# Kernel tuning notes

Hardware: AMD Instinct MI355X
Metric: run time of the kernel (lower is better)

Reference implementation:

```python
import jax, jax.numpy as jnp
import numpy as np

VX, VY = 0.16, 0.16
X_OFFSET = VX / 2 + 0.0      # vx/2 + offset[0]
Y_OFFSET = VY / 2 + (-39.68) # vy/2 + offset[1]
BN_EPS = 1e-5
V, P, C_IN, C_OUT = 40000, 32, 4, 64


def setup_inputs() -> dict:
    key = jax.random.key(0)
    k0, k1, k2, k3 = jax.random.split(key, 4)
    voxels = jax.random.normal(k0, (V, P, C_IN), dtype=jnp.float32)
    num_point_per_voxel = jnp.maximum(
        jax.random.randint(k1, (V,), 0, P + 1), 1).astype(jnp.int32)
    coors = jax.random.randint(k2, (V, 2), 0, 400).astype(jnp.int32)
    W = jax.random.normal(k3, (C_OUT, C_IN + 5), dtype=jnp.float32) * 0.1
    gamma = jnp.ones((C_OUT,), dtype=jnp.float32)
    beta = jnp.zeros((C_OUT,), dtype=jnp.float32)
    return {"voxels": voxels, "num_point_per_voxel": num_point_per_voxel,
            "coors": coors, "W": W, "gamma": gamma, "beta": beta}


def reference(voxels, num_point_per_voxel, coors, W, gamma, beta):
    npts = num_point_per_voxel.astype(voxels.dtype)  # [V]
    xyz = voxels[:, :, :3]
    # cluster offset: subtract per-pillar mean of valid points
    points_mean = jnp.sum(xyz, axis=1, keepdims=True) / npts[:, None, None]
    f_cluster = xyz - points_mean  # [V, P, 3]
    # pillar-center offset
    cx = coors[:, 0].astype(voxels.dtype) * VX + X_OFFSET  # [V]
    cy = coors[:, 1].astype(voxels.dtype) * VY + Y_OFFSET
    f_center = jnp.stack([voxels[:, :, 0] - cx[:, None],
                          voxels[:, :, 1] - cy[:, None]], axis=-1)  # [V, P, 2]
    features = jnp.concatenate([voxels, f_cluster, f_center], axis=-1)  # [V, P, 9]
    # zero out padded points
    point_ids = jnp.arange(P, dtype=jnp.int32)[None, :]
    mask = (num_point_per_voxel[:, None] > point_ids).astype(features.dtype)
    features = features * mask[:, :, None]
    # 1x1 conv == per-point linear: [V, P, 9] x [64, 9] -> [V, P, 64]
    x = jnp.einsum('vpc,oc->vpo', features, W)
    # BatchNorm1d (train mode): stats over (voxel, point) dims per channel
    mean = jnp.mean(x, axis=(0, 1))
    var = jnp.var(x, axis=(0, 1))
    x = (x - mean) * jax.lax.rsqrt(var + BN_EPS) * gamma + beta
    x = jax.nn.relu(x)
    # max over points -> [V, 64]
    return jnp.max(x, axis=1)
```

## Files before the change

kernel.cpp:

```cpp
#include <hip/hip_runtime.h>
#include <hip/hip_bf16.h>

#define V_N   40000
#define P_N   32
#define NTOT  (V_N * P_N)
#define VXc   0.16f
#define VYc   0.16f
#define XOFF  0.08f
#define YOFF  (-39.6f)
#define BN_EPS 1e-5f

#define SBLK  250
#define PBLK  2500
#define NSHARD 8
#define CNT_BYTES  (54 * NSHARD * 32 * 4)
#define MEANS_OFF  57344
#define CY_OFF     (MEANS_OFF + V_N * 16)

#define FOR_S(X) X(0) X(1) X(2) X(3) X(4) X(5) X(6) X(7) X(8)
#define FOR_M(X) \
  X(0,0) X(0,1) X(0,2) X(0,3) X(0,4) X(0,5) X(0,6) X(0,7) X(0,8) \
  X(1,1) X(1,2) X(1,3) X(1,4) X(1,5) X(1,6) X(1,7) X(1,8) \
  X(2,2) X(2,3) X(2,4) X(2,5) X(2,6) X(2,7) X(2,8) \
  X(3,3) X(3,4) X(3,5) X(3,6) X(3,7) X(3,8) \
  X(4,4) X(4,5) X(4,6) X(4,7) X(4,8) \
  X(5,5) X(5,6) X(5,7) X(5,8) \
  X(6,6) X(6,7) X(6,8) \
  X(7,7) X(7,8) \
  X(8,8)

__device__ __forceinline__ float wave_sum(float x) {
#pragma unroll
    for (int m = 1; m < 64; m <<= 1) x += __shfl_xor(x, m, 64);
    return x;
}

__device__ __forceinline__ float rdlane(float x, int l) {
    return __uint_as_float(__builtin_amdgcn_readlane(__float_as_uint(x), l));
}

#define DECL_S(i)   float S##i = 0.f;
#define DECL_M(i,j) float M##i##_##j = 0.f;
#define ACC_S(i)    S##i += f##i;
#define ACC_M(i,j)  M##i##_##j = fmaf(f##i, f##j, M##i##_##j);
#define RED_S(i)    S##i = wave_sum(S##i);
#define RED_M(i,j)  M##i##_##j = wave_sum(M##i##_##j);
#define ST_S(i)     r[k++] = S##i;
#define ST_M(i,j)   r[k++] = M##i##_##j;

#define STAT_BODY(q, v)                                                       \
        {                                                                     \
            float sx = q.x, sy = q.y, sz = q.z;                               \
            _Pragma("unroll")                                                 \
            for (int m = 1; m < 32; m <<= 1) {                                \
                sx += __shfl_xor(sx, m, 64);                                  \
                sy += __shfl_xor(sy, m, 64);                                  \
                sz += __shfl_xor(sz, m, 64);                                  \
            }                                                                 \
            const int   npts = npts_arr[v];                                   \
            const float inv  = 1.f / (float)npts;                             \
            const float mx = sx * inv, my = sy * inv, mz = sz * inv;          \
            const float cx = (float)coors[2 * (v)]     * VXc + XOFF;          \
            const float cy = (float)coors[2 * (v) + 1] * VYc + YOFF;          \
            if (p == 0) { means[v] = make_float4(mx, my, mz, cx);             \
                          cyv[v] = cy; }                                      \
            const float g  = (p < npts) ? 1.f : 0.f;                          \
            const float f0 = q.x * g;                                         \
            const float f1 = q.y * g;                                         \
            const float f2 = q.z * g;                                         \
            const float f3 = q.w * g;                                         \
            const float f4 = (q.x - mx) * g;                                  \
            const float f5 = (q.y - my) * g;                                  \
            const float f6 = (q.z - mz) * g;                                  \
            const float f7 = (q.x - cx) * g;                                  \
            const float f8 = (q.y - cy) * g;                                  \
            FOR_S(ACC_S)                                                      \
            FOR_M(ACC_M)                                                      \
        }

__global__ __launch_bounds__(256) void stats_kernel(
    const float4* __restrict__ voxels,
    const int*    __restrict__ npts_arr,
    const int*    __restrict__ coors,
    float*        __restrict__ ws)
{
    float*  cnt   = ws;
    float4* means = (float4*)((char*)ws + MEANS_OFF);
    float*  cyv   = (float*)((char*)ws + CY_OFF);

    const int lane = threadIdx.x & 63;
    const int p    = lane & 31;
    const int half = lane >> 5;
    const int gw   = (blockIdx.x * 256 + threadIdx.x) >> 6;
    const int nw   = (SBLK * 256) >> 6;

    FOR_S(DECL_S)
    FOR_M(DECL_M)

    for (int vb = gw * 4; vb < V_N; vb += nw * 4) {
        const int vA = vb + half;
        const int vB = vb + 2 + half;
        float4 q1 = voxels[(size_t)vA * P_N + p];
        float4 q2 = voxels[(size_t)vB * P_N + p];
        STAT_BODY(q1, vA)
        STAT_BODY(q2, vB)
    }

    FOR_S(RED_S)
    FOR_M(RED_M)

    __shared__ float red[4][54];
    const int wib = threadIdx.x >> 6;
    if (lane == 0) {
        float* r = red[wib];
        int k = 0;
        FOR_S(ST_S)
        FOR_M(ST_M)
    }
    __syncthreads();
    if (threadIdx.x < 54) {
        float s = red[0][threadIdx.x] + red[1][threadIdx.x]
                + red[2][threadIdx.x] + red[3][threadIdx.x];
        atomicAdd(&cnt[(threadIdx.x * NSHARD + (blockIdx.x & (NSHARD - 1))) * 32], s);
    }
}

__global__ __launch_bounds__(256) void pfn_kernel(
    const float4* __restrict__ voxels,
    const int*    __restrict__ npts_arr,
    const float*  __restrict__ W,
    const float*  __restrict__ gamma,
    const float*  __restrict__ beta,
    const float*  __restrict__ ws,
    float*        __restrict__ out)
{
    const float*  cnt   = ws;
    const float4* means = (const float4*)((const char*)ws + MEANS_OFF);
    const float*  cyv   = (const float*)((const char*)ws + CY_OFF);

    __shared__ float stc[54];
    __shared__ float affs[10][64];

    const int lane = threadIdx.x & 63;
    const int wib  = threadIdx.x >> 6;

    if (threadIdx.x < 54) {
        float s = 0.f;
#pragma unroll
        for (int sh = 0; sh < NSHARD; ++sh)
            s += cnt[(threadIdx.x * NSHARD + sh) * 32];
        stc[threadIdx.x] = s;
    }
    __syncthreads();
    if (threadIdx.x < 64) {
        const int o = threadIdx.x;
        float w[9];
#pragma unroll
        for (int c = 0; c < 9; ++c) w[c] = W[o * 9 + c];

        const float invN = 1.f / (float)NTOT;
        float mean = 0.f;
#pragma unroll
        for (int c = 0; c < 9; ++c) mean = fmaf(w[c], stc[c], mean);
        mean *= invN;

        float ex2 = 0.f;
        int k = 9;
#pragma unroll
        for (int i = 0; i < 9; ++i)
#pragma unroll
            for (int j = i; j < 9; ++j) {
                const float coef = (i == j) ? 1.f : 2.f;
                ex2 = fmaf(coef * w[i] * w[j], stc[k], ex2);
                ++k;
            }
        ex2 *= invN;
        const float var   = ex2 - mean * mean;
        const float scale = gamma[o] * rsqrtf(var + BN_EPS);
        const float bias  = fmaf(-mean, scale, beta[o]);

        affs[0][o] = (w[0] + w[4] + w[7]) * scale;
        affs[1][o] = (w[1] + w[5] + w[8]) * scale;
        affs[2][o] = (w[2] + w[6]) * scale;
        affs[3][o] =  w[3] * scale;
        affs[4][o] =  w[4] * scale;
        affs[5][o] =  w[5] * scale;
        affs[6][o] =  w[6] * scale;
        affs[7][o] =  w[7] * scale;
        affs[8][o] =  w[8] * scale;
        affs[9][o] =  bias;
    }
    __syncthreads();

    const float a0   = affs[0][lane];
    const float a1   = affs[1][lane];
    const float a2   = affs[2][lane];
    const float a3   = affs[3][lane];
    const float u4   = affs[4][lane];
    const float u5   = affs[5][lane];
    const float u6   = affs[6][lane];
    const float u7   = affs[7][lane];
    const float u8   = affs[8][lane];
    const float bias = affs[9][lane];

    const int gwave = blockIdx.x * 4 + wib;

#define DOT(P_, OFS_) \
    fmaf(rdlane(q.x, (P_) + (OFS_)), a0, \
    fmaf(rdlane(q.y, (P_) + (OFS_)), a1, \
    fmaf(rdlane(q.z, (P_) + (OFS_)), a2, \
         rdlane(q.w, (P_) + (OFS_)) * a3)))

#pragma unroll
    for (int it = 0; it < 2; ++it) {
        const int vA = gwave * 4 + it * 2;
        const int vB = vA + 1;

        const int vv = vA + (lane >> 5);
        const float4 q = voxels[(size_t)vv * P_N + (lane & 31)];

        const int nA = __builtin_amdgcn_readfirstlane(npts_arr[vA]);
        const int nB = __builtin_amdgcn_readfirstlane(npts_arr[vB]);

        const float4 mA = means[vA];
        const float4 mB = means[vB];
        const float cyA = cyv[vA];
        const float cyB = cyv[vB];

        const float bA = -fmaf(mA.x, u4, fmaf(mA.y, u5, fmaf(mA.z, u6,
                           fmaf(mA.w, u7, cyA * u8))));
        const float bB = -fmaf(mB.x, u4, fmaf(mB.y, u5, fmaf(mB.z, u6,
                           fmaf(mB.w, u7, cyB * u8))));

        float e0 = -3.4e38f, e1 = -3.4e38f;
        {
            int pp = 0;
            for (; pp + 1 < nA; pp += 2) {
                const float d0 = DOT(pp, 0);
                const float d1 = DOT(pp + 1, 0);
                e0 = fmaxf(e0, d0);
                e1 = fmaxf(e1, d1);
            }
            if (pp < nA) e0 = fmaxf(e0, DOT(pp, 0));
        }
        float mfA = fmaxf(e0, e1) + bA;
        if (nA < P_N) mfA = fmaxf(mfA, 0.f);
        out[(size_t)vA * 64 + lane] = fmaxf(mfA + bias, 0.f);

        float g0 = -3.4e38f, g1 = -3.4e38f;
        {
            int pp = 0;
            for (; pp + 1 < nB; pp += 2) {
                const float d0 = DOT(pp, 32);
                const float d1 = DOT(pp + 1, 32);
                g0 = fmaxf(g0, d0);
                g1 = fmaxf(g1, d1);
            }
            if (pp < nB) g0 = fmaxf(g0, DOT(pp, 32));
        }
        float mfB = fmaxf(g0, g1) + bB;
        if (nB < P_N) mfB = fmaxf(mfB, 0.f);
        out[(size_t)vB * 64 + lane] = fmaxf(mfB + bias, 0.f);
    }
#undef DOT
}

extern "C" void kernel_launch(void* const* d_in, const int* in_sizes, int n_in,
                              void* d_out, int out_size, void* d_ws, size_t ws_size,
                              hipStream_t stream)
{
    const float4* voxels = (const float4*)d_in[0];
    const int*    npts   = (const int*)d_in[1];
    const int*    coors  = (const int*)d_in[2];
    const float*  W      = (const float*)d_in[3];
    const float*  gamma  = (const float*)d_in[4];
    const float*  beta   = (const float*)d_in[5];
    float*        out    = (float*)d_out;
    float*        ws     = (float*)d_ws;

    hipMemsetAsync(d_ws, 0, CNT_BYTES, stream);
    stats_kernel<<<SBLK, 256, 0, stream>>>(voxels, npts, coors, ws);
    pfn_kernel  <<<PBLK, 256, 0, stream>>>(voxels, npts, W, gamma, beta, ws, out);
}
```

Measured before the change: 115.7 us.

## Use DPP row ops for wave reductions and double stats grid and shards

Replaces the shfl_xor butterfly reductions in the stats kernel with DPP row-shift/broadcast sequences plus readlane, both for the per-voxel 32-lane mean and for the final 64-lane reductions of the 54 moment sums. The stats grid is doubled to 500 blocks and the atomic shard count to 16, with the workspace offsets moved to fit the larger count buffer. This aims to cut ds_bpermute/LDS traffic in the reductions and to raise parallelism, at the cost of more partial sums to combine and depending on correct DPP control encodings.

```diff
diff --git a/kernel.cpp b/kernel.cpp
--- a/kernel.cpp
+++ b/kernel.cpp
@@ -10,11 +10,11 @@
 #define YOFF  (-39.6f)
 #define BN_EPS 1e-5f
 
-#define SBLK  250
+#define SBLK  500
 #define PBLK  2500
-#define NSHARD 8
+#define NSHARD 16
 #define CNT_BYTES  (54 * NSHARD * 32 * 4)
-#define MEANS_OFF  57344
+#define MEANS_OFF  131072
 #define CY_OFF     (MEANS_OFF + V_N * 16)
 
 #define FOR_S(X) X(0) X(1) X(2) X(3) X(4) X(5) X(6) X(7) X(8)
@@ -29,37 +29,53 @@
   X(7,7) X(7,8) \
   X(8,8)
 
-__device__ __forceinline__ float wave_sum(float x) {
-#pragma unroll
-    for (int m = 1; m < 64; m <<= 1) x += __shfl_xor(x, m, 64);
-    return x;
-}
-
 __device__ __forceinline__ float rdlane(float x, int l) {
     return __uint_as_float(__builtin_amdgcn_readlane(__float_as_uint(x), l));
+}
+
+template <int CTRL>
+__device__ __forceinline__ float dpp0(float x) {
+    return __int_as_float(__builtin_amdgcn_update_dpp(
+        0, __float_as_int(x), CTRL, 0xF, 0xF, true));
+}
+
+__device__ __forceinline__ float half_sum32(float x, bool hi) {
+    x += dpp0<0x111>(x);
+    x += dpp0<0x112>(x);
+    x += dpp0<0x114>(x);
+    x += dpp0<0x118>(x);
+    x += dpp0<0x142>(x);
+    const float a = rdlane(x, 31);
+    const float b = rdlane(x, 63);
+    return hi ? b : a;
+}
+
+__device__ __forceinline__ float full_sum64(float x) {
+    x += dpp0<0x111>(x);
+    x += dpp0<0x112>(x);
+    x += dpp0<0x114>(x);
+    x += dpp0<0x118>(x);
+    x += dpp0<0x142>(x);
+    x += dpp0<0x143>(x);
+    return rdlane(x, 63);
 }
 
 #define DECL_S(i)   float S##i = 0.f;
 #define DECL_M(i,j) float M##i##_##j = 0.f;
 #define ACC_S(i)    S##i += f##i;
 #define ACC_M(i,j)  M##i##_##j = fmaf(f##i, f##j, M##i##_##j);
-#define RED_S(i)    S##i = wave_sum(S##i);
-#define RED_M(i,j)  M##i##_##j = wave_sum(M##i##_##j);
+#define RED_S(i)    S##i = full_sum64(S##i);
+#define RED_M(i,j)  M##i##_##j = full_sum64(M##i##_##j);
 #define ST_S(i)     r[k++] = S##i;
 #define ST_M(i,j)   r[k++] = M##i##_##j;
 
 #define STAT_BODY(q, v)                                                       \
         {                                                                     \
-            float sx = q.x, sy = q.y, sz = q.z;                               \
-            _Pragma("unroll")                                                 \
-            for (int m = 1; m < 32; m <<= 1) {                                \
-                sx += __shfl_xor(sx, m, 64);                                  \
-                sy += __shfl_xor(sy, m, 64);                                  \
-                sz += __shfl_xor(sz, m, 64);                                  \
-            }                                                                 \
             const int   npts = npts_arr[v];                                   \
             const float inv  = 1.f / (float)npts;                             \
-            const float mx = sx * inv, my = sy * inv, mz = sz * inv;          \
+            const float mx = half_sum32(q.x, hi) * inv;                       \
+            const float my = half_sum32(q.y, hi) * inv;                       \
+            const float mz = half_sum32(q.z, hi) * inv;                       \
             const float cx = (float)coors[2 * (v)]     * VXc + XOFF;          \
             const float cy = (float)coors[2 * (v) + 1] * VYc + YOFF;          \
             if (p == 0) { means[v] = make_float4(mx, my, mz, cx);             \
@@ -88,11 +104,12 @@
     float4* means = (float4*)((char*)ws + MEANS_OFF);
     float*  cyv   = (float*)((char*)ws + CY_OFF);
 
-    const int lane = threadIdx.x & 63;
-    const int p    = lane & 31;
-    const int half = lane >> 5;
-    const int gw   = (blockIdx.x * 256 + threadIdx.x) >> 6;
-    const int nw   = (SBLK * 256) >> 6;
+    const int  lane = threadIdx.x & 63;
+    const int  p    = lane & 31;
+    const int  half = lane >> 5;
+    const bool hi   = lane >= 32;
+    const int  gw   = (blockIdx.x * 256 + threadIdx.x) >> 6;
+    const int  nw   = (SBLK * 256) >> 6;
 
     FOR_S(DECL_S)
     FOR_M(DECL_M)
```

Result: faster. 113.0 us (-2.3%).
